# Kernel optimization log

Hardware: AMD Instinct MI355X
Metric: run time of the kernel (lower is better)

## Reference

```python
import jax, jax.numpy as jnp
import numpy as np

N, E, G = 50000, 250000, 512
I_DIM, H, E_DIM = 32, 32, 16


def setup_inputs() -> dict:
    key = jax.random.key(0)
    ks = jax.random.split(key, 16)
    f32 = jnp.float32

    def w(k, shape, fan_in):
        return (jax.random.normal(k, shape, f32) / np.float32(np.sqrt(fan_in)))

    return {
        "x": jax.random.normal(ks[0], (N, I_DIM), f32),
        "edge_attr": jax.random.normal(ks[1], (E, E_DIM), f32),
        "edge_index": jax.random.randint(ks[2], (2, E), 0, N),
        "batch": jnp.sort(jax.random.randint(ks[3], (N,), 0, G)),
        "alpha": jnp.float32(1.0),
        # lin0
        "W0": w(ks[4], (I_DIM, H), I_DIM), "b0": jnp.zeros((H,), f32),
        # NNConv edge-weight MLP: Linear(e,h) -> ReLU -> Linear(h, h*h)
        "We1": w(ks[5], (E_DIM, H), E_DIM), "be1": jnp.zeros((H,), f32),
        "We2": w(ks[6], (H, H * H), H) * 0.1, "be2": jnp.zeros((H * H,), f32),
        # NNConv root weight + bias
        "Wroot": w(ks[7], (H, H), H), "bconv": jnp.zeros((H,), f32),
        # GRU (torch layout: gates [r,z,n] stacked -> 3H rows)
        "Wih": w(ks[8], (3 * H, H), H), "bih": jnp.zeros((3 * H,), f32),
        "Whh": w(ks[9], (3 * H, H), H), "bhh": jnp.zeros((3 * H,), f32),
        # lin1 head (label)
        "W1a": w(ks[10], (H, H), H), "b1a": jnp.zeros((H,), f32),
        "W1b": w(ks[11], (H, 1), H), "b1b": jnp.zeros((1,), f32),
        # lin2 head (domain)
        "W2a": w(ks[12], (H, H), H), "b2a": jnp.zeros((H,), f32),
        "W2b": w(ks[13], (H, 2), H), "b2b": jnp.zeros((2,), f32),
    }


def _segment_mean(vals, ids, num_segments):
    s = jax.ops.segment_sum(vals, ids, num_segments=num_segments)
    cnt = jax.ops.segment_sum(jnp.ones((vals.shape[0], 1), vals.dtype), ids,
                              num_segments=num_segments)
    return s / jnp.maximum(cnt, 1.0)


def reference(x, edge_attr, edge_index, batch, alpha,
              W0, b0, We1, be1, We2, be2, Wroot, bconv,
              Wih, bih, Whh, bhh, W1a, b1a, W1b, b1b, W2a, b2a, W2b, b2b):
    n_nodes = x.shape[0]
    src, dst = edge_index[0], edge_index[1]

    # lin0
    out = jax.nn.relu(x @ W0 + b0)          # [N, H]
    h = out                                   # GRU hidden (single layer, 1 step)

    # edge MLP -> per-edge [H, H] weights (constant across the 3 iterations)
    ew = jax.nn.relu(edge_attr @ We1 + be1) @ We2 + be2   # [E, H*H]
    ew = ew.reshape(-1, H, H)                              # [E, H, H]

    for _ in range(3):
        # NNConv: gather source states, per-edge matmul, scatter-mean to dst
        msg = jnp.einsum('eh,eho->eo', out[src], ew)       # [E, H]
        agg = _segment_mean(msg, dst, n_nodes)             # [N, H]
        m = jax.nn.relu(agg + out @ Wroot + bconv)         # [N, H]
        # GRU step (torch gate order r, z, n)
        gi = m @ Wih.T + bih
        gh = h @ Whh.T + bhh
        r = jax.nn.sigmoid(gi[:, :H] + gh[:, :H])
        z = jax.nn.sigmoid(gi[:, H:2 * H] + gh[:, H:2 * H])
        n = jnp.tanh(gi[:, 2 * H:] + r * gh[:, 2 * H:])
        h = (1.0 - z) * n + z * h
        out = h

    # gradient reversal is identity in forward
    num_graphs = G
    pooled = _segment_mean(out, batch, num_graphs)          # [G, H]

    label_out = (jax.nn.relu(pooled @ W1a + b1a) @ W1b + b1b).reshape(-1)  # [G]
    domain_out = jax.nn.relu(pooled @ W2a + b2a) @ W2b + b2b               # [G, 2]
    return label_out, jax.nn.log_softmax(domain_out, axis=1)
```

## Files before the change

### kernel.cpp

```cpp
#include <hip/hip_runtime.h>

typedef unsigned short u16;
typedef unsigned int u32;

#define NN 50000
#define EE 250000
#define GG 512

typedef __bf16 bf16x8 __attribute__((ext_vector_type(8)));
typedef float  f32x4  __attribute__((ext_vector_type(4)));

__device__ __forceinline__ u16 f2bfu(float f) {
    __bf16 b = (__bf16)f; u16 u; __builtin_memcpy(&u, &b, 2); return u;
}
__device__ __forceinline__ float sigf(float x) { return 1.f / (1.f + expf(-x)); }

__global__ void prep_B(const float* __restrict__ We2, const float* __restrict__ be2,
                       u16* __restrict__ Bg) {
    int idx = blockIdx.x * blockDim.x + threadIdx.x;
    if (idx >= 33 * 1024) return;
    int kk = idx >> 10, off = idx & 1023;
    int ct = off >> 9, l = (off >> 3) & 63, j = off & 7;
    int q = l >> 4, c = l & 15, o = c + 16 * ct;
    float v;
    if (kk < 32) v = We2[(32 * kk + 8 * q + j) * 32 + o];
    else         v = be2[(8 * q + j) * 32 + o];
    Bg[idx] = f2bfu(v);
}

__global__ void prep_WT(const float* __restrict__ Wih, const float* __restrict__ Whh,
                        float4* __restrict__ wta, float2* __restrict__ wtb) {
    int t = blockIdx.x * blockDim.x + threadIdx.x;
    if (t >= 1024) return;
    int k = t >> 5, j = t & 31;
    wta[t] = make_float4(Wih[j * 32 + k], Wih[(32 + j) * 32 + k],
                         Wih[(64 + j) * 32 + k], Whh[j * 32 + k]);
    wtb[t] = make_float2(Whh[(32 + j) * 32 + k], Whh[(64 + j) * 32 + k]);
}

__global__ void hist_k(const int* __restrict__ ei, const int* __restrict__ batch,
                       int* __restrict__ degc, int* __restrict__ gcnt) {
    int i = blockIdx.x * blockDim.x + threadIdx.x;
    if (i < EE) atomicAdd(degc + ei[EE + i], 1);
    if (i < NN) atomicAdd(gcnt + batch[i], 1);
}

__global__ __launch_bounds__(512) void scan_blk_k(const int* __restrict__ degc,
                                                  int* __restrict__ cursor,
                                                  int* __restrict__ bsum) {
    __shared__ int s[512];
    int tid = threadIdx.x, i = blockIdx.x * 512 + tid;
    int v = (i < NN) ? degc[i] : 0;
    s[tid] = v; __syncthreads();
#pragma unroll
    for (int off = 1; off < 512; off <<= 1) {
        int t2 = (tid >= off) ? s[tid - off] : 0;
        __syncthreads();
        s[tid] += t2;
        __syncthreads();
    }
    if (i < NN) cursor[i] = s[tid] - v;
    if (tid == 511) bsum[blockIdx.x] = s[511];
}

__global__ void scan_top_k(const int* __restrict__ bsum, int* __restrict__ boffs) {
    __shared__ int s[128];
    int tid = threadIdx.x;
    int v = (tid < 98) ? bsum[tid] : 0;
    s[tid] = v; __syncthreads();
#pragma unroll
    for (int off = 1; off < 128; off <<= 1) {
        int t2 = (tid >= off) ? s[tid - off] : 0;
        __syncthreads();
        s[tid] += t2;
        __syncthreads();
    }
    if (tid < 98) boffs[tid] = s[tid] - v;
}

__global__ __launch_bounds__(512) void scan_fix_k(int* __restrict__ cursor,
                                                  const int* __restrict__ boffs,
                                                  const int* __restrict__ degc,
                                                  float* __restrict__ dinv) {
    int i = blockIdx.x * 512 + threadIdx.x;
    if (i >= NN) return;
    cursor[i] += boffs[i >> 9];
    int c = degc[i];
    dinv[i] = 1.f / (float)(c > 0 ? c : 1);
}

__global__ void scatter_k(const int* __restrict__ ei, int* __restrict__ cursor,
                          int* __restrict__ posOf, int* __restrict__ srcs,
                          int* __restrict__ dsts) {
    int e = blockIdx.x * blockDim.x + threadIdx.x;
    if (e >= EE) return;
    int d = ei[EE + e];
    int p = atomicAdd(cursor + d, 1);
    posOf[e] = p;
    srcs[p] = ei[e];
    dsts[p] = d;
}

__global__ void prep_edges(const float* __restrict__ ea, const float* __restrict__ We1,
                           const float* __restrict__ be1, const int* __restrict__ posOf,
                           u16* __restrict__ tmat) {
    int e = blockIdx.x * blockDim.x + threadIdx.x;
    if (e >= EE) return;
    const float4* ep = (const float4*)(ea + (size_t)e * 16);
    float a[16];
#pragma unroll
    for (int i = 0; i < 4; i++) {
        float4 v = ep[i];
        a[4 * i] = v.x; a[4 * i + 1] = v.y; a[4 * i + 2] = v.z; a[4 * i + 3] = v.w;
    }
    u32 outw[16];
#pragma unroll
    for (int p = 0; p < 16; p++) {
        float acc0 = be1[2 * p], acc1 = be1[2 * p + 1];
#pragma unroll
        for (int k = 0; k < 16; k++) {
            acc0 += a[k] * We1[k * 32 + 2 * p];
            acc1 += a[k] * We1[k * 32 + 2 * p + 1];
        }
        acc0 = fmaxf(acc0, 0.f); acc1 = fmaxf(acc1, 0.f);
        outw[p] = (u32)f2bfu(acc0) | ((u32)f2bfu(acc1) << 16);
    }
    uint4* op = (uint4*)(tmat + (size_t)posOf[e] * 32);
#pragma unroll
    for (int i = 0; i < 4; i++)
        op[i] = make_uint4(outw[4 * i], outw[4 * i + 1], outw[4 * i + 2], outw[4 * i + 3]);
}

__global__ void lin0_k(const float* __restrict__ x, const float* __restrict__ W0,
                       const float* __restrict__ b0, float* __restrict__ hf,
                       u16* __restrict__ cur) {
    int n = blockIdx.x * blockDim.x + threadIdx.x;
    if (n >= NN) return;
    const float4* xp = (const float4*)(x + (size_t)n * 32);
    float a[32];
#pragma unroll
    for (int i = 0; i < 8; i++) {
        float4 v = xp[i];
        a[4 * i] = v.x; a[4 * i + 1] = v.y; a[4 * i + 2] = v.z; a[4 * i + 3] = v.w;
    }
    float o[32];
#pragma unroll 4
    for (int c = 0; c < 32; c++) {
        float acc = b0[c];
#pragma unroll
        for (int k = 0; k < 32; k++) acc += a[k] * W0[k * 32 + c];
        o[c] = fmaxf(acc, 0.f);
    }
    float4* hp = (float4*)(hf + (size_t)n * 32);
#pragma unroll
    for (int i = 0; i < 8; i++) hp[i] = make_float4(o[4 * i], o[4 * i + 1], o[4 * i + 2], o[4 * i + 3]);
    uint4* cp = (uint4*)(cur + (size_t)n * 32);
#pragma unroll
    for (int i = 0; i < 4; i++) {
        u32 p0 = (u32)f2bfu(o[8 * i + 0]) | ((u32)f2bfu(o[8 * i + 1]) << 16);
        u32 p1 = (u32)f2bfu(o[8 * i + 2]) | ((u32)f2bfu(o[8 * i + 3]) << 16);
        u32 p2 = (u32)f2bfu(o[8 * i + 4]) | ((u32)f2bfu(o[8 * i + 5]) << 16);
        u32 p3 = (u32)f2bfu(o[8 * i + 6]) | ((u32)f2bfu(o[8 * i + 7]) << 16);
        cp[i] = make_uint4(p0, p1, p2, p3);
    }
}

__global__ __launch_bounds__(512) void msg_k(const u16* __restrict__ cur,
                                             const u16* __restrict__ tmat,
                                             const int* __restrict__ srcs,
                                             const int* __restrict__ dsts,
                                             const u16* __restrict__ Bg,
                                             float* __restrict__ agg) {
    __shared__ uint4 Bl[4096];
    const uint4* Bgv = (const uint4*)Bg;
    for (int i = threadIdx.x; i < 4096; i += 512) Bl[i] = Bgv[i];
    __syncthreads();
    const u16* Bl16 = (const u16*)Bl;

    int l = threadIdx.x & 63;
    int q = l >> 4, r = l & 15;
    int wid = (blockIdx.x * blockDim.x + threadIdx.x) >> 6;
    int nw  = (gridDim.x * blockDim.x) >> 6;

    for (int tile = wid; tile < EE / 16; tile += nw) {
        int eb = tile * 16;
        int srow = srcs[eb + r];
        bf16x8 sv = *reinterpret_cast<const bf16x8*>(cur + (size_t)srow * 32 + q * 8);
        float sf[8];
#pragma unroll
        for (int j = 0; j < 8; j++) sf[j] = (float)sv[j];
        const uint4* tp = reinterpret_cast<const uint4*>(tmat + (size_t)(eb + r) * 32);
        f32x4 acc0 = {0.f, 0.f, 0.f, 0.f}, acc1 = {0.f, 0.f, 0.f, 0.f};
#pragma unroll
        for (int kq = 0; kq < 4; kq++) {
            uint4 tw4 = tp[kq];
            u32 tws[4] = {tw4.x, tw4.y, tw4.z, tw4.w};
#pragma unroll
            for (int du = 0; du < 4; du++) {
                u32 w = tws[du];
#pragma unroll
                for (int hl = 0; hl < 2; hl++) {
                    int kk = kq * 8 + du * 2 + hl;
                    float tf = __uint_as_float(hl ? (w & 0xffff0000u) : (w << 16));
                    bf16x8 av;
#pragma unroll
                    for (int j = 0; j < 8; j++) av[j] = (__bf16)(tf * sf[j]);
                    bf16x8 b0 = *reinterpret_cast<const bf16x8*>(Bl16 + kk * 1024 + l * 8);
                    bf16x8 b1 = *reinterpret_cast<const bf16x8*>(Bl16 + kk * 1024 + 512 + l * 8);
                    acc0 = __builtin_amdgcn_mfma_f32_16x16x32_bf16(av, b0, acc0, 0, 0, 0);
                    acc1 = __builtin_amdgcn_mfma_f32_16x16x32_bf16(av, b1, acc1, 0, 0, 0);
                }
            }
        }
        {
            bf16x8 b0 = *reinterpret_cast<const bf16x8*>(Bg + 32 * 1024 + l * 8);
            bf16x8 b1 = *reinterpret_cast<const bf16x8*>(Bg + 32 * 1024 + 512 + l * 8);
            acc0 = __builtin_amdgcn_mfma_f32_16x16x32_bf16(sv, b0, acc0, 0, 0, 0);
            acc1 = __builtin_amdgcn_mfma_f32_16x16x32_bf16(sv, b1, acc1, 0, 0, 0);
        }
        {
            int d0 = dsts[eb + 4 * q + 0], d1 = dsts[eb + 4 * q + 1];
            int d2 = dsts[eb + 4 * q + 2], d3 = dsts[eb + 4 * q + 3];
            float ca = acc0[0], cb = acc1[0];
            if (d0 != d1) {
                atomicAdd(agg + (size_t)d0 * 32 + r, ca);
                atomicAdd(agg + (size_t)d0 * 32 + 16 + r, cb);
                ca = 0.f; cb = 0.f;
            }
            ca += acc0[1]; cb += acc1[1];
            if (d1 != d2) {
                atomicAdd(agg + (size_t)d1 * 32 + r, ca);
                atomicAdd(agg + (size_t)d1 * 32 + 16 + r, cb);
                ca = 0.f; cb = 0.f;
            }
            ca += acc0[2]; cb += acc1[2];
            if (d2 != d3) {
                atomicAdd(agg + (size_t)d2 * 32 + r, ca);
                atomicAdd(agg + (size_t)d2 * 32 + 16 + r, cb);
                ca = 0.f; cb = 0.f;
            }
            ca += acc0[3]; cb += acc1[3];
            atomicAdd(agg + (size_t)d3 * 32 + r, ca);
            atomicAdd(agg + (size_t)d3 * 32 + 16 + r, cb);
        }
    }
}

__global__ __launch_bounds__(512) void node_update_v4(
        float* __restrict__ hf, u16* __restrict__ cur,
        const float* __restrict__ agg, const float* __restrict__ dinv,
        const float* __restrict__ Wroot, const float* __restrict__ bconv,
        const float4* __restrict__ wta_g, const float2* __restrict__ wtb_g,
        const float* __restrict__ bih, const float* __restrict__ bhh) {
    __shared__ float  wroot_l[1024];
    __shared__ float4 wta_l[1024];
    __shared__ float2 wtb_l[1024];
    __shared__ float  h_l[32 * 66];
    __shared__ float  m_l[32 * 66];
    __shared__ float  bias_l[192];

    const int t = threadIdx.x;
    const int w = t >> 6;
    const int lane = t & 63;
    const int nb = blockIdx.x * 64;
    const int n = nb + lane;
    const int nc = (n < NN) ? n : (NN - 1);

    if (t < 256) ((float4*)wroot_l)[t] = ((const float4*)Wroot)[t];
    wta_l[t] = wta_g[t]; wta_l[t + 512] = wta_g[t + 512];
    ((float4*)wtb_l)[t] = ((const float4*)wtb_g)[t];
    if (t < 192) bias_l[t] = (t < 96) ? bih[t] : bhh[t - 96];

    {
        const int nl = t >> 3, ch = t & 7;
        const int ng = nb + nl;
        const int ngc = (ng < NN) ? ng : (NN - 1);
        float4 v = *(const float4*)(hf + (size_t)ngc * 32 + ch * 4);
        h_l[(ch * 4 + 0) * 66 + nl] = v.x;
        h_l[(ch * 4 + 1) * 66 + nl] = v.y;
        h_l[(ch * 4 + 2) * 66 + nl] = v.z;
        h_l[(ch * 4 + 3) * 66 + nl] = v.w;
    }
    __syncthreads();

    const int c0 = w * 4;
    {
        const float di = dinv[nc];
        float4 ag = *(const float4*)(agg + (size_t)nc * 32 + c0);
        float a0 = bconv[c0 + 0] + ag.x * di;
        float a1 = bconv[c0 + 1] + ag.y * di;
        float a2 = bconv[c0 + 2] + ag.z * di;
        float a3 = bconv[c0 + 3] + ag.w * di;
#pragma unroll 4
        for (int k = 0; k < 32; k++) {
            float hk = h_l[k * 66 + lane];
            float4 wr = *(const float4*)&wroot_l[k * 32 + c0];
            a0 = fmaf(hk, wr.x, a0); a1 = fmaf(hk, wr.y, a1);
            a2 = fmaf(hk, wr.z, a2); a3 = fmaf(hk, wr.w, a3);
        }
        m_l[(c0 + 0) * 66 + lane] = fmaxf(a0, 0.f);
        m_l[(c0 + 1) * 66 + lane] = fmaxf(a1, 0.f);
        m_l[(c0 + 2) * 66 + lane] = fmaxf(a2, 0.f);
        m_l[(c0 + 3) * 66 + lane] = fmaxf(a3, 0.f);
    }
    __syncthreads();

    float outv[4];
#pragma unroll
    for (int half = 0; half < 2; half++) {
        const int j0 = c0 + half * 2;
        float air0 = 0.f, aiz0 = 0.f, ain0 = 0.f, ahr0 = 0.f, ahz0 = 0.f, ahn0 = 0.f;
        float air1 = 0.f, aiz1 = 0.f, ain1 = 0.f, ahr1 = 0.f, ahz1 = 0.f, ahn1 = 0.f;
#pragma unroll 4
        for (int k = 0; k < 32; k++) {
            float mk = m_l[k * 66 + lane];
            float hk = h_l[k * 66 + lane];
            float4 wa0 = wta_l[k * 32 + j0];
            float2 wb0 = wtb_l[k * 32 + j0];
            float4 wa1 = wta_l[k * 32 + j0 + 1];
            float2 wb1 = wtb_l[k * 32 + j0 + 1];
            air0 = fmaf(mk, wa0.x, air0); aiz0 = fmaf(mk, wa0.y, aiz0);
            ain0 = fmaf(mk, wa0.z, ain0); ahr0 = fmaf(hk, wa0.w, ahr0);
            ahz0 = fmaf(hk, wb0.x, ahz0); ahn0 = fmaf(hk, wb0.y, ahn0);
            air1 = fmaf(mk, wa1.x, air1); aiz1 = fmaf(mk, wa1.y, aiz1);
            ain1 = fmaf(mk, wa1.z, ain1); ahr1 = fmaf(hk, wa1.w, ahr1);
            ahz1 = fmaf(hk, wb1.x, ahz1); ahn1 = fmaf(hk, wb1.y, ahn1);
        }
#pragma unroll
        for (int jj = 0; jj < 2; jj++) {
            const int j = j0 + jj;
            float air = jj ? air1 : air0, aiz = jj ? aiz1 : aiz0, ain = jj ? ain1 : ain0;
            float ahr = jj ? ahr1 : ahr0, ahz = jj ? ahz1 : ahz0, ahn = jj ? ahn1 : ahn0;
            float r = sigf(air + ahr + bias_l[j] + bias_l[96 + j]);
            float z = sigf(aiz + ahz + bias_l[32 + j] + bias_l[128 + j]);
            float g = tanhf(ain + bias_l[64 + j] + r * (ahn + bias_l[160 + j]));
            float ho = h_l[j * 66 + lane];
            outv[half * 2 + jj] = (1.f - z) * g + z * ho;
        }
    }
    __syncthreads();

#pragma unroll
    for (int i = 0; i < 4; i++) m_l[(c0 + i) * 66 + lane] = outv[i];
    __syncthreads();

    {
        const int nl = t >> 3, q = (t & 7) * 4;
        const int ng = nb + nl;
        if (ng < NN) {
            float4 v = make_float4(m_l[(q + 0) * 66 + nl], m_l[(q + 1) * 66 + nl],
                                   m_l[(q + 2) * 66 + nl], m_l[(q + 3) * 66 + nl]);
            *(float4*)(hf + (size_t)ng * 32 + q) = v;
            u32 p0 = (u32)f2bfu(v.x) | ((u32)f2bfu(v.y) << 16);
            u32 p1 = (u32)f2bfu(v.z) | ((u32)f2bfu(v.w) << 16);
            *(uint2*)(cur + (size_t)ng * 32 + q) = make_uint2(p0, p1);
        }
    }
}

__global__ __launch_bounds__(256) void pool_k2(const float* __restrict__ hf,
                                               const int* __restrict__ batch,
                                               float* __restrict__ gsum) {
    int wv = (blockIdx.x * 256 + threadIdx.x) >> 6;
    int lane = threadIdx.x & 63;
    int sub = lane >> 5, o = lane & 31;
    int base = wv * 256;
    if (base >= NN) return;
    float acc = 0.f; int gcur = -1;
#pragma unroll 4
    for (int i = 0; i < 128; i++) {
        int n = base + 2 * i + sub;
        if (n < NN) {
            int g = batch[n];
            float v = hf[(size_t)n * 32 + o];
            if (g != gcur) {
                if (gcur >= 0) atomicAdd(gsum + gcur * 32 + o, acc);
                gcur = g; acc = v;
            } else {
                acc += v;
            }
        }
    }
    if (gcur >= 0) atomicAdd(gsum + gcur * 32 + o, acc);
}

__global__ void head_k(const float* __restrict__ gsum, const int* __restrict__ gcnt,
                       const float* __restrict__ W1a, const float* __restrict__ b1a,
                       const float* __restrict__ W1b, const float* __restrict__ b1b,
                       const float* __restrict__ W2a, const float* __restrict__ b2a,
                       const float* __restrict__ W2b, const float* __restrict__ b2b,
                       float* __restrict__ dout) {
    int g = blockIdx.x * blockDim.x + threadIdx.x;
    if (g >= GG) return;
    int c0 = gcnt[g];
    float rc = 1.f / (float)(c0 > 0 ? c0 : 1);
    float p[32];
#pragma unroll
    for (int i = 0; i < 32; i++) p[i] = gsum[g * 32 + i] * rc;
    float lab = b1b[0];
#pragma unroll 4
    for (int c = 0; c < 32; c++) {
        float acc = b1a[c];
#pragma unroll
        for (int k = 0; k < 32; k++) acc += p[k] * W1a[k * 32 + c];
        lab += fmaxf(acc, 0.f) * W1b[c];
    }
    float d0 = b2b[0], d1 = b2b[1];
#pragma unroll 4
    for (int c = 0; c < 32; c++) {
        float acc = b2a[c];
#pragma unroll
        for (int k = 0; k < 32; k++) acc += p[k] * W2a[k * 32 + c];
        float t = fmaxf(acc, 0.f);
        d0 += t * W2b[c * 2];
        d1 += t * W2b[c * 2 + 1];
    }
    float mx = fmaxf(d0, d1);
    float ls = mx + logf(expf(d0 - mx) + expf(d1 - mx));
    dout[g] = lab;
    dout[GG + g * 2]     = d0 - ls;
    dout[GG + g * 2 + 1] = d1 - ls;
}

extern "C" void kernel_launch(void* const* d_in, const int* in_sizes, int n_in,
                              void* d_out, int out_size, void* d_ws, size_t ws_size,
                              hipStream_t stream) {
    const float* x   = (const float*)d_in[0];
    const float* ea  = (const float*)d_in[1];
    const int* ei    = (const int*)d_in[2];
    const int* batch = (const int*)d_in[3];
    const float* W0 = (const float*)d_in[5],  *b0 = (const float*)d_in[6];
    const float* We1 = (const float*)d_in[7], *be1 = (const float*)d_in[8];
    const float* We2 = (const float*)d_in[9], *be2 = (const float*)d_in[10];
    const float* Wroot = (const float*)d_in[11], *bconv = (const float*)d_in[12];
    const float* Wih = (const float*)d_in[13], *bih = (const float*)d_in[14];
    const float* Whh = (const float*)d_in[15], *bhh = (const float*)d_in[16];
    const float* W1a = (const float*)d_in[17], *b1a = (const float*)d_in[18];
    const float* W1b = (const float*)d_in[19], *b1b = (const float*)d_in[20];
    const float* W2a = (const float*)d_in[21], *b2a = (const float*)d_in[22];
    const float* W2b = (const float*)d_in[23], *b2b = (const float*)d_in[24];
    float* dout = (float*)d_out;

    char* w = (char*)d_ws;
    u16*   tmat = (u16*)w;    w += (size_t)EE * 32 * 2;
    u16*   Bg   = (u16*)w;    w += 33 * 1024 * 2 + 512;
    float* hf   = (float*)w;  w += (size_t)NN * 32 * 4;
    u16*   cur  = (u16*)w;    w += (size_t)NN * 32 * 2;
    float* agg  = (float*)w;  w += (size_t)NN * 32 * 4;
    float* dinv = (float*)w;  w += 200192;
    int*   degc = (int*)w;    w += 200192;
    float* gsum = (float*)w;  w += (size_t)GG * 32 * 4;
    int*   gcnt = (int*)w;    w += 2048;
    float4* wta_g = (float4*)w; w += 1024 * 16;
    float2* wtb_g = (float2*)w; w += 1024 * 8;
    int*   cursor = (int*)w;  w += 200192;
    int*   posOf  = (int*)w;  w += (size_t)EE * 4;
    int*   srcs   = (int*)w;  w += (size_t)EE * 4;
    int*   dsts   = (int*)w;  w += (size_t)EE * 4;
    int*   bsum   = (int*)w;  w += 512;
    int*   boffs  = (int*)w;  w += 512;

    hipMemsetAsync(degc, 0, NN * 4, stream);
    hipMemsetAsync(gcnt, 0, GG * 4, stream);
    hipMemsetAsync(gsum, 0, GG * 32 * 4, stream);

    hist_k<<<(EE + 255) / 256, 256, 0, stream>>>(ei, batch, degc, gcnt);
    scan_blk_k<<<98, 512, 0, stream>>>(degc, cursor, bsum);
    scan_top_k<<<1, 128, 0, stream>>>(bsum, boffs);
    scan_fix_k<<<98, 512, 0, stream>>>(cursor, boffs, degc, dinv);
    scatter_k<<<(EE + 255) / 256, 256, 0, stream>>>(ei, cursor, posOf, srcs, dsts);

    prep_B<<<132, 256, 0, stream>>>(We2, be2, Bg);
    prep_WT<<<4, 256, 0, stream>>>(Wih, Whh, wta_g, wtb_g);
    prep_edges<<<(EE + 255) / 256, 256, 0, stream>>>(ea, We1, be1, posOf, tmat);
    lin0_k<<<(NN + 255) / 256, 256, 0, stream>>>(x, W0, b0, hf, cur);

    for (int it = 0; it < 3; it++) {
        hipMemsetAsync(agg, 0, (size_t)NN * 32 * 4, stream);
        msg_k<<<512, 512, 0, stream>>>(cur, tmat, srcs, dsts, Bg, agg);
        node_update_v4<<<(NN + 63) / 64, 512, 0, stream>>>(hf, cur, agg, dinv,
                                                           Wroot, bconv, wta_g, wtb_g, bih, bhh);
    }

    pool_k2<<<49, 256, 0, stream>>>(hf, batch, gsum);
    head_k<<<2, 256, 0, stream>>>(gsum, gcnt, W1a, b1a, W1b, b1b, W2a, b2a, W2b, b2b, dout);
}
```

Before: 638.8 us.

## Replace atomic scatter-add with CSR segmented reduction over stored messages

The message kernel now writes per-edge messages (sorted by destination) to a dense fp32 buffer, and a new reduce kernel sums each node's contiguous CSR range using row starts computed during the scan. This removes the float atomics and the per-iteration memset of agg, and makes the aggregation deterministic. In exchange it adds a 32 MB write and read of messages per iteration plus an extra kernel launch.

Result: faster. 618.3 us (-3.2%).

```diff
diff --git a/kernel.cpp b/kernel.cpp
--- a/kernel.cpp
+++ b/kernel.cpp
@@ -81,24 +81,26 @@
 __global__ __launch_bounds__(512) void scan_fix_k(int* __restrict__ cursor,
                                                   const int* __restrict__ boffs,
                                                   const int* __restrict__ degc,
-                                                  float* __restrict__ dinv) {
+                                                  float* __restrict__ dinv,
+                                                  int* __restrict__ rs) {
     int i = blockIdx.x * 512 + threadIdx.x;
     if (i >= NN) return;
-    cursor[i] += boffs[i >> 9];
+    int v = cursor[i] + boffs[i >> 9];
+    cursor[i] = v;
+    rs[i] = v;
+    if (i == NN - 1) rs[NN] = EE;
     int c = degc[i];
     dinv[i] = 1.f / (float)(c > 0 ? c : 1);
 }
 
 __global__ void scatter_k(const int* __restrict__ ei, int* __restrict__ cursor,
-                          int* __restrict__ posOf, int* __restrict__ srcs,
-                          int* __restrict__ dsts) {
+                          int* __restrict__ posOf, int* __restrict__ srcs) {
     int e = blockIdx.x * blockDim.x + threadIdx.x;
     if (e >= EE) return;
     int d = ei[EE + e];
     int p = atomicAdd(cursor + d, 1);
     posOf[e] = p;
     srcs[p] = ei[e];
-    dsts[p] = d;
 }
 
 __global__ void prep_edges(const float* __restrict__ ea, const float* __restrict__ We1,
@@ -168,9 +170,8 @@
 __global__ __launch_bounds__(512) void msg_k(const u16* __restrict__ cur,
                                              const u16* __restrict__ tmat,
                                              const int* __restrict__ srcs,
-                                             const int* __restrict__ dsts,
                                              const u16* __restrict__ Bg,
-                                             float* __restrict__ agg) {
+                                             float* __restrict__ msgf) {
     __shared__ uint4 Bl[4096];
     const uint4* Bgv = (const uint4*)Bg;
     for (int i = threadIdx.x; i < 4096; i += 512) Bl[i] = Bgv[i];
@@ -219,31 +220,34 @@
             acc1 = __builtin_amdgcn_mfma_f32_16x16x32_bf16(sv, b1, acc1, 0, 0, 0);
         }
         {
-            int d0 = dsts[eb + 4 * q + 0], d1 = dsts[eb + 4 * q + 1];
-            int d2 = dsts[eb + 4 * q + 2], d3 = dsts[eb + 4 * q + 3];
-            float ca = acc0[0], cb = acc1[0];
-            if (d0 != d1) {
-                atomicAdd(agg + (size_t)d0 * 32 + r, ca);
-                atomicAdd(agg + (size_t)d0 * 32 + 16 + r, cb);
-                ca = 0.f; cb = 0.f;
+            float* mp = msgf + (size_t)eb * 32;
+#pragma unroll
+            for (int j = 0; j < 4; j++) {
+                mp[(4 * q + j) * 32 + r]      = acc0[j];
+                mp[(4 * q + j) * 32 + 16 + r] = acc1[j];
             }
-            ca += acc0[1]; cb += acc1[1];
-            if (d1 != d2) {
-                atomicAdd(agg + (size_t)d1 * 32 + r, ca);
-                atomicAdd(agg + (size_t)d1 * 32 + 16 + r, cb);
-                ca = 0.f; cb = 0.f;
-            }
-            ca += acc0[2]; cb += acc1[2];
-            if (d2 != d3) {
-                atomicAdd(agg + (size_t)d2 * 32 + r, ca);
-                atomicAdd(agg + (size_t)d2 * 32 + 16 + r, cb);
-                ca = 0.f; cb = 0.f;
-            }
-            ca += acc0[3]; cb += acc1[3];
-            atomicAdd(agg + (size_t)d3 * 32 + r, ca);
-            atomicAdd(agg + (size_t)d3 * 32 + 16 + r, cb);
-        }
-    }
+        }
+    }
+}
+
+__global__ __launch_bounds__(256) void reduce_k(const float* __restrict__ msgf,
+                                                const int* __restrict__ rs,
+                                                float* __restrict__ agg) {
+    int t = blockIdx.x * 256 + threadIdx.x;
+    int n = t >> 2, qd = t & 3;
+    if (n >= NN) return;
+    int p0 = rs[n], p1 = rs[n + 1];
+    float a0 = 0.f, a1 = 0.f, a2 = 0.f, a3 = 0.f;
+    float b0 = 0.f, b1 = 0.f, b2 = 0.f, b3 = 0.f;
+    for (int p = p0; p < p1; p++) {
+        const float4* mp = (const float4*)(msgf + (size_t)p * 32 + qd * 8);
+        float4 v0 = mp[0], v1 = mp[1];
+        a0 += v0.x; a1 += v0.y; a2 += v0.z; a3 += v0.w;
+        b0 += v1.x; b1 += v1.y; b2 += v1.z; b3 += v1.w;
+    }
+    float4* ap = (float4*)(agg + (size_t)n * 32 + qd * 8);
+    ap[0] = make_float4(a0, a1, a2, a3);
+    ap[1] = make_float4(b0, b1, b2, b3);
 }
 
 __global__ __launch_bounds__(512) void node_update_v4(
@@ -456,9 +460,10 @@
     int*   cursor = (int*)w;  w += 200192;
     int*   posOf  = (int*)w;  w += (size_t)EE * 4;
     int*   srcs   = (int*)w;  w += (size_t)EE * 4;
-    int*   dsts   = (int*)w;  w += (size_t)EE * 4;
+    int*   rs     = (int*)w;  w += 200192;
     int*   bsum   = (int*)w;  w += 512;
     int*   boffs  = (int*)w;  w += 512;
+    float* msgf   = (float*)w; w += (size_t)EE * 32 * 4;
 
     hipMemsetAsync(degc, 0, NN * 4, stream);
     hipMemsetAsync(gcnt, 0, GG * 4, stream);
@@ -467,8 +472,8 @@
     hist_k<<<(EE + 255) / 256, 256, 0, stream>>>(ei, batch, degc, gcnt);
     scan_blk_k<<<98, 512, 0, stream>>>(degc, cursor, bsum);
     scan_top_k<<<1, 128, 0, stream>>>(bsum, boffs);
-    scan_fix_k<<<98, 512, 0, stream>>>(cursor, boffs, degc, dinv);
-    scatter_k<<<(EE + 255) / 256, 256, 0, stream>>>(ei, cursor, posOf, srcs, dsts);
+    scan_fix_k<<<98, 512, 0, stream>>>(cursor, boffs, degc, dinv, rs);
+    scatter_k<<<(EE + 255) / 256, 256, 0, stream>>>(ei, cursor, posOf, srcs);
 
     prep_B<<<132, 256, 0, stream>>>(We2, be2, Bg);
     prep_WT<<<4, 256, 0, stream>>>(Wih, Whh, wta_g, wtb_g);
@@ -476,8 +481,8 @@
     lin0_k<<<(NN + 255) / 256, 256, 0, stream>>>(x, W0, b0, hf, cur);
 
     for (int it = 0; it < 3; it++) {
-        hipMemsetAsync(agg, 0, (size_t)NN * 32 * 4, stream);
-        msg_k<<<512, 512, 0, stream>>>(cur, tmat, srcs, dsts, Bg, agg);
+        msg_k<<<512, 512, 0, stream>>>(cur, tmat, srcs, Bg, msgf);
+        reduce_k<<<(4 * NN + 255) / 256, 256, 0, stream>>>(msgf, rs, agg);
         node_update_v4<<<(NN + 63) / 64, 512, 0, stream>>>(hf, cur, agg, dinv,
                                                            Wroot, bconv, wta_g, wtb_g, bih, bhh);
     }
```
